# Kernel tuning notes

Measured on AMD Instinct MI355X. Metric: run time of the kernel, lower is better.

The kernel has to match this reference:

```python
import jax, jax.numpy as jnp
import numpy as np

DIM = 256
NUM_HEADS = 8
HEAD_DIM = DIM // NUM_HEADS
SCALE = HEAD_DIM ** -0.5
KSIZE = 5


def setup_inputs() -> dict:
    key = jax.random.key(0)
    ks = jax.random.split(key, 6)
    B, C, H, W = 8, DIM, 32, 32
    x = jax.random.normal(ks[0], (B, C, H, W), dtype=jnp.float32)
    qkv_w = jax.random.normal(ks[1], (3 * C, C), dtype=jnp.float32) * 0.02  # 1x1 conv, no bias
    proj_w = jax.random.normal(ks[2], (C, C), dtype=jnp.float32) * 0.02    # 1x1 conv
    proj_b = jax.random.normal(ks[3], (C,), dtype=jnp.float32) * 0.02
    lepe_w = jax.random.normal(ks[4], (C, 1, KSIZE, KSIZE), dtype=jnp.float32) * 0.02  # depthwise
    lepe_b = jax.random.normal(ks[5], (C,), dtype=jnp.float32) * 0.02
    return {"x": x, "qkv_w": qkv_w, "proj_w": proj_w, "proj_b": proj_b,
            "lepe_w": lepe_w, "lepe_b": lepe_b}


def _forward(x, qkv_w, proj_w, proj_b, lepe_w, lepe_b):
    B, C, H, W = x.shape
    N = H * W
    # 1x1 conv qkv: [B,3C,H,W]
    qkv = jnp.einsum('bchw,oc->bohw', x, qkv_w)
    q, k, v = jnp.split(qkv, 3, axis=1)
    # reshape to [B, heads, head_dim, N]
    qh = q.reshape(B, NUM_HEADS, HEAD_DIM, N)
    kh = k.reshape(B, NUM_HEADS, HEAD_DIM, N)
    vh = v.reshape(B, NUM_HEADS, HEAD_DIM, N)
    # attn = (q^T k) * scale, softmax over keys -> [B, heads, N, N]
    attn = jnp.einsum('bhdn,bhdm->bhnm', qh, kh)
    attn = jax.nn.softmax(attn * SCALE, axis=-1)
    # out = attn @ v^T -> [B, heads, N, head_dim] -> [B, C, H, W]
    out = jnp.einsum('bhnm,bhdm->bhdn', attn, vh).reshape(B, C, H, W)
    # LePE: depthwise conv on v (image layout) + residual add
    lepe = jax.lax.conv_general_dilated(
        v, lepe_w, window_strides=(1, 1),
        padding=[(KSIZE // 2, KSIZE // 2)] * 2,
        dimension_numbers=('NCHW', 'OIHW', 'NCHW'),
        feature_group_count=C) + lepe_b[None, :, None, None]
    out = out + lepe
    # 1x1 proj
    out = jnp.einsum('bchw,oc->bohw', out, proj_w) + proj_b[None, :, None, None]
    return out


def reference(x, qkv_w, proj_w, proj_b, lepe_w, lepe_b):
    return _forward(x, qkv_w, proj_w, proj_b, lepe_w, lepe_b)
```

## Files before the change

### kernel.cpp

```cpp
#include <hip/hip_runtime.h>

#define NB 8
#define NC 256
#define NN 1024

typedef unsigned short u16;
typedef unsigned int u32;
typedef __attribute__((ext_vector_type(8))) short short8;
typedef __attribute__((ext_vector_type(4))) float f32x4;

__device__ __forceinline__ u16 f2b(float f){ union{float ff;u32 i;}v; v.ff=f; u32 r=v.i+0x7FFFu+((v.i>>16)&1u); return (u16)(r>>16); }
__device__ __forceinline__ float b2f(u16 p){ union{u32 i;float f;}v; v.i=((u32)p)<<16; return v.f; }

#define QSC 0.25503486f

union FR { uint4 u; short8 s; };

__global__ void __launch_bounds__(256) k_castw(const float* __restrict__ qkvw,
                                               const float* __restrict__ projw,
                                               u16* __restrict__ wb){
  const int idx = blockIdx.x*256 + threadIdx.x;
  const float* src = (idx < 49152) ? (qkvw + (size_t)idx*4)
                                   : (projw + (size_t)(idx-49152)*4);
  float4 a = *(const float4*)src;
  uint2 o;
  o.x = (u32)f2b(a.x) | ((u32)f2b(a.y)<<16);
  o.y = (u32)f2b(a.z) | ((u32)f2b(a.w)<<16);
  *(uint2*)(wb + (size_t)idx*4) = o;
}

__global__ void __launch_bounds__(256) k_castx(const float* __restrict__ x,
                                               u16* __restrict__ xt){
  const int n0 = blockIdx.x*64, c0 = blockIdx.y*128, b = blockIdx.z;
  const int tid = threadIdx.x;
  __shared__ u16 lt[64][136];
  #pragma unroll
  for (int cc = 0; cc < 4; cc++){
    const int c = c0 + cc*32 + (tid>>3);
    const int ns = (tid&7)*8;
    const float* src = x + ((size_t)(b*NC + c))*NN + n0 + ns;
    float4 a = *(const float4*)src;
    float4 d = *(const float4*)(src+4);
    const int cl = c - c0;
    lt[ns+0][cl] = f2b(a.x); lt[ns+1][cl] = f2b(a.y);
    lt[ns+2][cl] = f2b(a.z); lt[ns+3][cl] = f2b(a.w);
    lt[ns+4][cl] = f2b(d.x); lt[ns+5][cl] = f2b(d.y);
    lt[ns+6][cl] = f2b(d.z); lt[ns+7][cl] = f2b(d.w);
  }
  __syncthreads();
  #pragma unroll
  for (int p = 0; p < 4; p++){
    const int flat = p*256 + tid;
    const int row = flat >> 4, seg = flat & 15;
    uint4 d = *(uint4*)&lt[row][seg*8];
    *(uint4*)(xt + ((size_t)(b*NN + n0 + row))*NC + c0 + seg*8) = d;
  }
}

__global__ void __launch_bounds__(256) k_qkv(const u16* __restrict__ wqb,
                                             const u16* __restrict__ xt,
                                             u16* __restrict__ qt,
                                             u16* __restrict__ kt,
                                             u16* __restrict__ v,
                                             u16* __restrict__ vt){
  const int ot = blockIdx.x, nt = blockIdx.y, b = blockIdx.z;
  const int o0 = ot*32;
  const int tid = threadIdx.x, wv = tid>>6, lane = tid&63;
  const int l15 = lane&15, quad = lane>>4;
  const int n0w = nt*256 + wv*64;
  __shared__ u16 swq[32][264];
  __shared__ u16 s2[4][64][40];
  #pragma unroll
  for (int i = 0; i < 4; i++){
    const int flat = i*256 + tid;
    const int row = flat >> 5, col = flat & 31;
    *(uint4*)&swq[row][col*8] = *(const uint4*)(wqb + (size_t)(o0+row)*NC + col*8);
  }
  __syncthreads();
  f32x4 acc[2][4];
  #pragma unroll
  for (int mt = 0; mt < 2; mt++)
    #pragma unroll
    for (int nt2 = 0; nt2 < 4; nt2++) acc[mt][nt2] = (f32x4){0.f,0.f,0.f,0.f};
  const u16* xb = xt + ((size_t)(b*NN + n0w))*NC;
  for (int k0 = 0; k0 < 256; k0 += 32){
    FR af[2], bf[4];
    af[0].u = *(uint4*)&swq[l15][k0 + quad*8];
    af[1].u = *(uint4*)&swq[16+l15][k0 + quad*8];
    #pragma unroll
    for (int nt2 = 0; nt2 < 4; nt2++)
      bf[nt2].u = *(const uint4*)(xb + (size_t)(nt2*16+l15)*NC + k0 + quad*8);
    #pragma unroll
    for (int mt = 0; mt < 2; mt++)
      #pragma unroll
      for (int nt2 = 0; nt2 < 4; nt2++)
        acc[mt][nt2] = __builtin_amdgcn_mfma_f32_16x16x32_bf16(af[mt].s, bf[nt2].s, acc[mt][nt2], 0,0,0);
  }
  if (ot < 16){
    const float sc = (ot < 8) ? QSC : 1.0f;
    u16* dstbase = (ot < 8) ? qt : kt;
    const int h = (ot < 8) ? ot : ot-8;
    #pragma unroll
    for (int mt = 0; mt < 2; mt++)
      #pragma unroll
      for (int nt2 = 0; nt2 < 4; nt2++){
        uint2 w;
        w.x = (u32)f2b(acc[mt][nt2][0]*sc) | ((u32)f2b(acc[mt][nt2][1]*sc)<<16);
        w.y = (u32)f2b(acc[mt][nt2][2]*sc) | ((u32)f2b(acc[mt][nt2][3]*sc)<<16);
        *(uint2*)&s2[wv][nt2*16+l15][mt*16+quad*4] = w;
      }
    __syncthreads();
    u16* db = dstbase + ((size_t)(b*8+h)*NN + n0w)*32;
    #pragma unroll
    for (int p = 0; p < 4; p++){
      const int n_loc = p*16 + (lane>>2), seg = lane&3;
      uint4 d = *(uint4*)&s2[wv][n_loc][seg*8];
      *(uint4*)(db + (size_t)n_loc*32 + seg*8) = d;
    }
  } else {
    const int c0 = o0 - 512;
    #pragma unroll
    for (int mt = 0; mt < 2; mt++)
      #pragma unroll
      for (int nt2 = 0; nt2 < 4; nt2++){
        #pragma unroll
        for (int r = 0; r < 4; r++)
          v[(size_t)(b*NC + c0 + mt*16 + quad*4 + r)*NN + n0w + nt2*16 + l15] = f2b(acc[mt][nt2][r]);
        uint2 w;
        w.x = (u32)f2b(acc[mt][nt2][0]) | ((u32)f2b(acc[mt][nt2][1])<<16);
        w.y = (u32)f2b(acc[mt][nt2][2]) | ((u32)f2b(acc[mt][nt2][3])<<16);
        *(uint2*)&s2[wv][nt2*16+l15][mt*16+quad*4] = w;
      }
    __syncthreads();
    u16* db = vt + ((size_t)(b*NN + n0w))*NC + c0;
    #pragma unroll
    for (int p = 0; p < 4; p++){
      const int n_loc = p*16 + (lane>>2), seg = lane&3;
      uint4 d = *(uint4*)&s2[wv][n_loc][seg*8];
      *(uint4*)(db + (size_t)n_loc*NC + seg*8) = d;
    }
  }
}

__global__ void __launch_bounds__(256) k_attn(const u16* __restrict__ qt,
                                              const u16* __restrict__ kt,
                                              const u16* __restrict__ v,
                                              u16* __restrict__ tt){
  const int h = blockIdx.y, b = blockIdx.z;
  const int tid = threadIdx.x;
  const int wv = tid >> 6, lane = tid & 63;
  const int l15 = lane & 15, quad = lane >> 4;
  const int bh = b*8 + h;
  const int q0 = (blockIdx.x*4 + wv)*32;

  __shared__ u16 pb[4][2][16][40];
  u16* pbA = &pb[wv][0][0][0];
  u16* pbB = &pb[wv][1][0][0];

  const u16* qtb = qt + (size_t)bh*NN*32;
  const u16* ktb = kt + (size_t)bh*NN*32;
  const u16* vbp = v + (size_t)(b*256 + h*32)*NN;

  FR qa, qb_;
  qa.u  = *(const uint4*)(qtb + (size_t)(q0      + l15)*32 + quad*8);
  qb_.u = *(const uint4*)(qtb + (size_t)(q0 + 16 + l15)*32 + quad*8);

  f32x4 z = {0.f,0.f,0.f,0.f};
  f32x4 oA0 = z, oA1 = z, oB0 = z, oB1 = z;
  float denA[4] = {0.f,0.f,0.f,0.f}, denB[4] = {0.f,0.f,0.f,0.f};

  for (int m0 = 0; m0 < NN; m0 += 32){
    FR kf0, kf1, vf0, vf1;
    kf0.u = *(const uint4*)(ktb + (size_t)(m0      + l15)*32 + quad*8);
    kf1.u = *(const uint4*)(ktb + (size_t)(m0 + 16 + l15)*32 + quad*8);
    vf0.u = *(const uint4*)(vbp + (size_t)(l15     )*NN + m0 + quad*8);
    vf1.u = *(const uint4*)(vbp + (size_t)(16 + l15)*NN + m0 + quad*8);

    f32x4 sA0 = __builtin_amdgcn_mfma_f32_16x16x32_bf16(qa.s,  kf0.s, z, 0,0,0);
    f32x4 sA1 = __builtin_amdgcn_mfma_f32_16x16x32_bf16(qa.s,  kf1.s, z, 0,0,0);
    f32x4 sB0 = __builtin_amdgcn_mfma_f32_16x16x32_bf16(qb_.s, kf0.s, z, 0,0,0);
    f32x4 sB1 = __builtin_amdgcn_mfma_f32_16x16x32_bf16(qb_.s, kf1.s, z, 0,0,0);

    #pragma unroll
    for (int r = 0; r < 4; r++){
      float pA0 = __builtin_amdgcn_exp2f(sA0[r]);
      float pA1 = __builtin_amdgcn_exp2f(sA1[r]);
      float pB0 = __builtin_amdgcn_exp2f(sB0[r]);
      float pB1 = __builtin_amdgcn_exp2f(sB1[r]);
      denA[r] += pA0 + pA1;
      denB[r] += pB0 + pB1;
      const int row = (quad*4 + r)*40;
      pbA[row + l15]      = (u16)(__float_as_uint(pA0)>>16);
      pbA[row + 16 + l15] = (u16)(__float_as_uint(pA1)>>16);
      pbB[row + l15]      = (u16)(__float_as_uint(pB0)>>16);
      pbB[row + 16 + l15] = (u16)(__float_as_uint(pB1)>>16);
    }
    FR pfA, pfB;
    pfA.u = *(const uint4*)(pbA + l15*40 + quad*8);
    pfB.u = *(const uint4*)(pbB + l15*40 + quad*8);

    oA0 = __builtin_amdgcn_mfma_f32_16x16x32_bf16(pfA.s, vf0.s, oA0, 0,0,0);
    oA1 = __builtin_amdgcn_mfma_f32_16x16x32_bf16(pfA.s, vf1.s, oA1, 0,0,0);
    oB0 = __builtin_amdgcn_mfma_f32_16x16x32_bf16(pfB.s, vf0.s, oB0, 0,0,0);
    oB1 = __builtin_amdgcn_mfma_f32_16x16x32_bf16(pfB.s, vf1.s, oB1, 0,0,0);
  }
  #pragma unroll
  for (int r = 0; r < 4; r++){
    #pragma unroll
    for (int m = 1; m < 16; m <<= 1){
      denA[r] += __shfl_xor(denA[r], m);
      denB[r] += __shfl_xor(denB[r], m);
    }
  }
  u16* tb = tt + ((size_t)(b*NN + q0))*NC + h*32;
  #pragma unroll
  for (int r = 0; r < 4; r++){
    const int q = quad*4 + r;
    const float iA = 1.f/denA[r], iB = 1.f/denB[r];
    tb[(size_t)q*NC + l15]           = f2b(oA0[r]*iA);
    tb[(size_t)q*NC + 16 + l15]      = f2b(oA1[r]*iA);
    tb[(size_t)(q+16)*NC + l15]      = f2b(oB0[r]*iB);
    tb[(size_t)(q+16)*NC + 16 + l15] = f2b(oB1[r]*iB);
  }
}

__global__ void __launch_bounds__(256) k_lepe(const u16* __restrict__ vt,
                                              const float* __restrict__ lw,
                                              const float* __restrict__ lb,
                                              u16* __restrict__ tt){
  const int b = blockIdx.y, c = threadIdx.x;
  const int n0 = blockIdx.x*8;
  const int y = n0 >> 5, x0 = n0 & 31;
  float wreg[25];
  #pragma unroll
  for (int i = 0; i < 25; i++) wreg[i] = lw[c*25+i];
  const float bias = lb[c];
  const u16* vb = vt + (size_t)(b*NN)*NC + c;
  u16* tb = tt + (size_t)(b*NN + n0)*NC + c;
  #pragma unroll
  for (int i = 0; i < 8; i++){
    float acc = bias;
    #pragma unroll
    for (int ky = 0; ky < 5; ky++){
      const int yy = y + ky - 2;
      if (yy < 0 || yy > 31) continue;
      #pragma unroll
      for (int kx = 0; kx < 5; kx++){
        const int xx = x0 + i + kx - 2;
        if (xx < 0 || xx > 31) continue;
        acc += wreg[ky*5+kx] * b2f(vb[(size_t)(yy*32+xx)*NC]);
      }
    }
    tb[(size_t)i*NC] = f2b(b2f(tb[(size_t)i*NC]) + acc);
  }
}

__global__ void __launch_bounds__(256) k_proj(const u16* __restrict__ wpb,
                                              const u16* __restrict__ tt,
                                              const float* __restrict__ pbias,
                                              float* __restrict__ out){
  const int ot = blockIdx.x, nt = blockIdx.y, b = blockIdx.z;
  const int o0 = ot*32;
  const int tid = threadIdx.x, wv = tid>>6, lane = tid&63;
  const int l15 = lane&15, quad = lane>>4;
  const int n0w = nt*256 + wv*64;
  __shared__ u16 swp[32][264];
  #pragma unroll
  for (int i = 0; i < 4; i++){
    const int flat = i*256 + tid;
    const int row = flat >> 5, col = flat & 31;
    *(uint4*)&swp[row][col*8] = *(const uint4*)(wpb + (size_t)(o0+row)*NC + col*8);
  }
  __syncthreads();
  f32x4 acc[2][4];
  #pragma unroll
  for (int mt = 0; mt < 2; mt++)
    #pragma unroll
    for (int nt2 = 0; nt2 < 4; nt2++) acc[mt][nt2] = (f32x4){0.f,0.f,0.f,0.f};
  const u16* tb = tt + ((size_t)(b*NN + n0w))*NC;
  for (int k0 = 0; k0 < 256; k0 += 32){
    FR af[2], bf[4];
    af[0].u = *(uint4*)&swp[l15][k0 + quad*8];
    af[1].u = *(uint4*)&swp[16+l15][k0 + quad*8];
    #pragma unroll
    for (int nt2 = 0; nt2 < 4; nt2++)
      bf[nt2].u = *(const uint4*)(tb + (size_t)(nt2*16+l15)*NC + k0 + quad*8);
    #pragma unroll
    for (int mt = 0; mt < 2; mt++)
      #pragma unroll
      for (int nt2 = 0; nt2 < 4; nt2++)
        acc[mt][nt2] = __builtin_amdgcn_mfma_f32_16x16x32_bf16(af[mt].s, bf[nt2].s, acc[mt][nt2], 0,0,0);
  }
  float bv[2][4];
  #pragma unroll
  for (int mt = 0; mt < 2; mt++)
    #pragma unroll
    for (int r = 0; r < 4; r++) bv[mt][r] = pbias[o0 + mt*16 + quad*4 + r];
  #pragma unroll
  for (int mt = 0; mt < 2; mt++)
    #pragma unroll
    for (int nt2 = 0; nt2 < 4; nt2++)
      #pragma unroll
      for (int r = 0; r < 4; r++)
        out[(size_t)(b*NC + o0 + mt*16 + quad*4 + r)*NN + n0w + nt2*16 + l15] = acc[mt][nt2][r] + bv[mt][r];
}

extern "C" void kernel_launch(void* const* d_in, const int* in_sizes, int n_in,
                              void* d_out, int out_size, void* d_ws, size_t ws_size,
                              hipStream_t stream){
  const float* x      = (const float*)d_in[0];
  const float* qkv_w  = (const float*)d_in[1];
  const float* proj_w = (const float*)d_in[2];
  const float* proj_b = (const float*)d_in[3];
  const float* lepe_w = (const float*)d_in[4];
  const float* lepe_b = (const float*)d_in[5];
  float* out = (float*)d_out;

  if (ws_size < (size_t)25690112) return;
  u16* wqb = (u16*)d_ws;
  u16* wpb = wqb + 196608;
  u16* xt  = wpb + 65536;
  u16* qt  = xt + 2097152;
  u16* kt  = qt + 2097152;
  u16* v   = kt + 2097152;
  u16* vt  = v  + 2097152;
  u16* tt  = vt + 2097152;

  k_castw<<<dim3(256),      256, 0, stream>>>(qkv_w, proj_w, wqb);
  k_castx<<<dim3(16, 2, 8), 256, 0, stream>>>(x, xt);
  k_qkv  <<<dim3(24, 4, 8), 256, 0, stream>>>(wqb, xt, qt, kt, v, vt);
  k_attn <<<dim3(8, 8, 8),  256, 0, stream>>>(qt, kt, v, tt);
  k_lepe <<<dim3(128, 8),   256, 0, stream>>>(vt, lepe_w, lepe_b, tt);
  k_proj <<<dim3(8, 4, 8),  256, 0, stream>>>(wpb, tt, proj_b, out);
}
```

Baseline: 146.5 us.

## Fuse LePE depthwise conv into attention epilogue and merge cast kernels

Moves the 5x5 depthwise LePE convolution into the attention kernel's epilogue. Each block stages its 4 image rows plus halo of v for its head into shared memory, and the conv result is added to the attention output before the single write to tt. This drops the separate transposed vt write from the qkv kernel and the read-modify-write of tt in a standalone LePE kernel. The two cast kernels are merged into one launch, for two fewer launches overall. In exchange the attention kernel uses more shared memory and registers, which may lower occupancy.

```diff
diff --git a/kernel.cpp b/kernel.cpp
--- a/kernel.cpp
+++ b/kernel.cpp
@@ -11,29 +11,33 @@
 
 __device__ __forceinline__ u16 f2b(float f){ union{float ff;u32 i;}v; v.ff=f; u32 r=v.i+0x7FFFu+((v.i>>16)&1u); return (u16)(r>>16); }
 __device__ __forceinline__ float b2f(u16 p){ union{u32 i;float f;}v; v.i=((u32)p)<<16; return v.f; }
+__device__ __forceinline__ float pklo(u32 p){ union{u32 i;float f;}v; v.i=p<<16; return v.f; }
+__device__ __forceinline__ float pkhi(u32 p){ union{u32 i;float f;}v; v.i=p&0xFFFF0000u; return v.f; }
 
 #define QSC 0.25503486f
 
 union FR { uint4 u; short8 s; };
 
-__global__ void __launch_bounds__(256) k_castw(const float* __restrict__ qkvw,
-                                               const float* __restrict__ projw,
-                                               u16* __restrict__ wb){
-  const int idx = blockIdx.x*256 + threadIdx.x;
-  const float* src = (idx < 49152) ? (qkvw + (size_t)idx*4)
-                                   : (projw + (size_t)(idx-49152)*4);
-  float4 a = *(const float4*)src;
-  uint2 o;
-  o.x = (u32)f2b(a.x) | ((u32)f2b(a.y)<<16);
-  o.y = (u32)f2b(a.z) | ((u32)f2b(a.w)<<16);
-  *(uint2*)(wb + (size_t)idx*4) = o;
-}
-
-__global__ void __launch_bounds__(256) k_castx(const float* __restrict__ x,
-                                               u16* __restrict__ xt){
-  const int n0 = blockIdx.x*64, c0 = blockIdx.y*128, b = blockIdx.z;
+__global__ void __launch_bounds__(256) k_cast(const float* __restrict__ qkvw,
+                                              const float* __restrict__ projw,
+                                              const float* __restrict__ x,
+                                              u16* __restrict__ wb,
+                                              u16* __restrict__ xt){
+  __shared__ u16 lt[64][136];
   const int tid = threadIdx.x;
-  __shared__ u16 lt[64][136];
+  if (blockIdx.x < 256){
+    const int idx = blockIdx.x*256 + tid;
+    const float* src = (idx < 49152) ? (qkvw + (size_t)idx*4)
+                                     : (projw + (size_t)(idx-49152)*4);
+    float4 a = *(const float4*)src;
+    uint2 o;
+    o.x = (u32)f2b(a.x) | ((u32)f2b(a.y)<<16);
+    o.y = (u32)f2b(a.z) | ((u32)f2b(a.w)<<16);
+    *(uint2*)(wb + (size_t)idx*4) = o;
+    return;
+  }
+  const int bx = blockIdx.x - 256;
+  const int n0 = (bx & 15)*64, c0 = ((bx>>4)&1)*128, b = bx>>5;
   #pragma unroll
   for (int cc = 0; cc < 4; cc++){
     const int c = c0 + cc*32 + (tid>>3);
@@ -61,8 +65,7 @@
                                              const u16* __restrict__ xt,
                                              u16* __restrict__ qt,
                                              u16* __restrict__ kt,
-                                             u16* __restrict__ v,
-                                             u16* __restrict__ vt){
+                                             u16* __restrict__ v){
   const int ot = blockIdx.x, nt = blockIdx.y, b = blockIdx.z;
   const int o0 = ot*32;
   const int tid = threadIdx.x, wv = tid>>6, lane = tid&63;
@@ -122,29 +125,18 @@
     #pragma unroll
     for (int mt = 0; mt < 2; mt++)
       #pragma unroll
-      for (int nt2 = 0; nt2 < 4; nt2++){
+      for (int nt2 = 0; nt2 < 4; nt2++)
         #pragma unroll
         for (int r = 0; r < 4; r++)
           v[(size_t)(b*NC + c0 + mt*16 + quad*4 + r)*NN + n0w + nt2*16 + l15] = f2b(acc[mt][nt2][r]);
-        uint2 w;
-        w.x = (u32)f2b(acc[mt][nt2][0]) | ((u32)f2b(acc[mt][nt2][1])<<16);
-        w.y = (u32)f2b(acc[mt][nt2][2]) | ((u32)f2b(acc[mt][nt2][3])<<16);
-        *(uint2*)&s2[wv][nt2*16+l15][mt*16+quad*4] = w;
-      }
-    __syncthreads();
-    u16* db = vt + ((size_t)(b*NN + n0w))*NC + c0;
-    #pragma unroll
-    for (int p = 0; p < 4; p++){
-      const int n_loc = p*16 + (lane>>2), seg = lane&3;
-      uint4 d = *(uint4*)&s2[wv][n_loc][seg*8];
-      *(uint4*)(db + (size_t)n_loc*NC + seg*8) = d;
-    }
   }
 }
 
 __global__ void __launch_bounds__(256) k_attn(const u16* __restrict__ qt,
                                               const u16* __restrict__ kt,
                                               const u16* __restrict__ v,
+                                              const float* __restrict__ lw,
+                                              const float* __restrict__ lb,
                                               u16* __restrict__ tt){
   const int h = blockIdx.y, b = blockIdx.z;
   const int tid = threadIdx.x;
@@ -154,8 +146,33 @@
   const int q0 = (blockIdx.x*4 + wv)*32;
 
   __shared__ u16 pb[4][2][16][40];
+  __shared__ u16 vstage[8][32][38];
+  __shared__ u16 s_out[4][32][36];
   u16* pbA = &pb[wv][0][0][0];
   u16* pbB = &pb[wv][1][0][0];
+
+  {
+    const int rr = tid >> 5, lc2 = tid & 31;
+    const int yy = blockIdx.x*4 - 2 + rr;
+    u32* dst32 = (u32*)&vstage[rr][lc2][0];
+    if (yy < 0 || yy > 31){
+      #pragma unroll
+      for (int j = 0; j < 19; j++) dst32[j] = 0;
+    } else {
+      const u16* src = v + ((size_t)(b*NC + h*32 + lc2))*NN + yy*32;
+      uint4 a = *(const uint4*)src;
+      uint4 b4 = *(const uint4*)(src+8);
+      uint4 c4 = *(const uint4*)(src+16);
+      uint4 d4 = *(const uint4*)(src+24);
+      dst32[0] = 0;
+      dst32[1]=a.x;  dst32[2]=a.y;  dst32[3]=a.z;  dst32[4]=a.w;
+      dst32[5]=b4.x; dst32[6]=b4.y; dst32[7]=b4.z; dst32[8]=b4.w;
+      dst32[9]=c4.x; dst32[10]=c4.y; dst32[11]=c4.z; dst32[12]=c4.w;
+      dst32[13]=d4.x; dst32[14]=d4.y; dst32[15]=d4.z; dst32[16]=d4.w;
+      dst32[17]=0; dst32[18]=0;
+    }
+  }
+  __syncthreads();
 
   const u16* qtb = qt + (size_t)bh*NN*32;
   const u16* ktb = kt + (size_t)bh*NN*32;
@@ -212,46 +229,48 @@
       denB[r] += __shfl_xor(denB[r], m);
     }
   }
-  u16* tb = tt + ((size_t)(b*NN + q0))*NC + h*32;
-  #pragma unroll
-  for (int r = 0; r < 4; r++){
-    const int q = quad*4 + r;
-    const float iA = 1.f/denA[r], iB = 1.f/denB[r];
-    tb[(size_t)q*NC + l15]           = f2b(oA0[r]*iA);
-    tb[(size_t)q*NC + 16 + l15]      = f2b(oA1[r]*iA);
-    tb[(size_t)(q+16)*NC + l15]      = f2b(oB0[r]*iB);
-    tb[(size_t)(q+16)*NC + 16 + l15] = f2b(oB1[r]*iB);
-  }
-}
-
-__global__ void __launch_bounds__(256) k_lepe(const u16* __restrict__ vt,
-                                              const float* __restrict__ lw,
-                                              const float* __restrict__ lb,
-                                              u16* __restrict__ tt){
-  const int b = blockIdx.y, c = threadIdx.x;
-  const int n0 = blockIdx.x*8;
-  const int y = n0 >> 5, x0 = n0 & 31;
-  float wreg[25];
-  #pragma unroll
-  for (int i = 0; i < 25; i++) wreg[i] = lw[c*25+i];
-  const float bias = lb[c];
-  const u16* vb = vt + (size_t)(b*NN)*NC + c;
-  u16* tb = tt + (size_t)(b*NN + n0)*NC + c;
-  #pragma unroll
-  for (int i = 0; i < 8; i++){
-    float acc = bias;
+  {
+    u16* so = &s_out[wv][0][0];
+    #pragma unroll
+    for (int r = 0; r < 4; r++){
+      const int q = quad*4 + r;
+      const float iA = 1.f/denA[r], iB = 1.f/denB[r];
+      so[q*36 + l15]           = f2b(oA0[r]*iA);
+      so[q*36 + 16 + l15]      = f2b(oA1[r]*iA);
+      so[(q+16)*36 + l15]      = f2b(oB0[r]*iB);
+      so[(q+16)*36 + 16 + l15] = f2b(oB1[r]*iB);
+    }
+  }
+  {
+    const int lc = lane & 31, qh = lane >> 5;
+    float lep[16];
+    const float lbias = lb[h*32 + lc];
+    #pragma unroll
+    for (int i = 0; i < 16; i++) lep[i] = lbias;
+    const float* lwc = lw + (size_t)(h*32 + lc)*25;
     #pragma unroll
     for (int ky = 0; ky < 5; ky++){
-      const int yy = y + ky - 2;
-      if (yy < 0 || yy > 31) continue;
-      #pragma unroll
-      for (int kx = 0; kx < 5; kx++){
-        const int xx = x0 + i + kx - 2;
-        if (xx < 0 || xx > 31) continue;
-        acc += wreg[ky*5+kx] * b2f(vb[(size_t)(yy*32+xx)*NC]);
+      const u32* vr = (const u32*)&vstage[wv + ky][lc][0];
+      float vv[20];
+      #pragma unroll
+      for (int jj = 0; jj < 10; jj++){
+        u32 pk = vr[qh*8 + jj];
+        vv[2*jj]   = pklo(pk);
+        vv[2*jj+1] = pkhi(pk);
       }
-    }
-    tb[(size_t)i*NC] = f2b(b2f(tb[(size_t)i*NC]) + acc);
+      const float w0 = lwc[ky*5+0], w1 = lwc[ky*5+1], w2 = lwc[ky*5+2],
+                  w3 = lwc[ky*5+3], w4 = lwc[ky*5+4];
+      #pragma unroll
+      for (int i = 0; i < 16; i++)
+        lep[i] += w0*vv[i] + w1*vv[i+1] + w2*vv[i+2] + w3*vv[i+3] + w4*vv[i+4];
+    }
+    u16* tb = tt + ((size_t)(b*NN + q0))*NC + h*32;
+    const u16* so = &s_out[wv][0][0];
+    #pragma unroll
+    for (int i = 0; i < 16; i++){
+      const int q = qh*16 + i;
+      tb[(size_t)q*NC + lc] = f2b(b2f(so[q*36 + lc]) + lep[i]);
+    }
   }
 }
 
@@ -316,20 +335,17 @@
   const float* lepe_b = (const float*)d_in[5];
   float* out = (float*)d_out;
 
-  if (ws_size < (size_t)25690112) return;
+  if (ws_size < (size_t)21495808) return;
   u16* wqb = (u16*)d_ws;
   u16* wpb = wqb + 196608;
   u16* xt  = wpb + 65536;
   u16* qt  = xt + 2097152;
   u16* kt  = qt + 2097152;
   u16* v   = kt + 2097152;
-  u16* vt  = v  + 2097152;
-  u16* tt  = vt + 2097152;
-
-  k_castw<<<dim3(256),      256, 0, stream>>>(qkv_w, proj_w, wqb);
-  k_castx<<<dim3(16, 2, 8), 256, 0, stream>>>(x, xt);
-  k_qkv  <<<dim3(24, 4, 8), 256, 0, stream>>>(wqb, xt, qt, kt, v, vt);
-  k_attn <<<dim3(8, 8, 8),  256, 0, stream>>>(qt, kt, v, tt);
-  k_lepe <<<dim3(128, 8),   256, 0, stream>>>(vt, lepe_w, lepe_b, tt);
-  k_proj <<<dim3(8, 4, 8),  256, 0, stream>>>(wpb, tt, proj_b, out);
-}
+  u16* tt  = v  + 2097152;
+
+  k_cast<<<dim3(512),     256, 0, stream>>>(qkv_w, proj_w, x, wqb, xt);
+  k_qkv <<<dim3(24, 4, 8),256, 0, stream>>>(wqb, xt, qt, kt, v);
+  k_attn<<<dim3(8, 8, 8), 256, 0, stream>>>(qt, kt, v, lepe_w, lepe_b, tt);
+  k_proj<<<dim3(8, 4, 8), 256, 0, stream>>>(wpb, tt, proj_b, out);
+}
```

Measured after the change: 121.8 us. 16.8% less time.
